# Kernel optimization log

Measured on AMD Instinct MI355X. Metric: run time of the kernel, lower is better.

Reference implementation:

```python
import jax, jax.numpy as jnp
import numpy as np

IOU_THRESHOLD = 0.5
NEGATIVE_RATIO = 3
ALPHA = 1.0
B, A, D, G = 64, 8732, 85, 32  # batch, anchors, 4+81 classes, max gt per image


def cxcywh_to_xyxy(b):
    cx, cy, w, h = b[..., 0], b[..., 1], b[..., 2], b[..., 3]
    return jnp.stack([cx - w / 2, cy - h / 2, cx + w / 2, cy + h / 2], axis=-1)


def box_iou(a, b):
    # a: (G,4) xyxy, b: (A,4) xyxy -> (G,A)
    lt = jnp.maximum(a[:, None, :2], b[None, :, :2])
    rb = jnp.minimum(a[:, None, 2:], b[None, :, 2:])
    wh = jnp.clip(rb - lt, 0.0)
    inter = wh[..., 0] * wh[..., 1]
    area_a = (a[:, 2] - a[:, 0]) * (a[:, 3] - a[:, 1])
    area_b = (b[:, 2] - b[:, 0]) * (b[:, 3] - b[:, 1])
    return inter / (area_a[:, None] + area_b[None, :] - inter)


def encode(gt, anchors):
    g_cxcy = (gt[:, :2] - anchors[:, :2]) / anchors[:, 2:]
    g_wh = jnp.log(gt[:, 2:]) - jnp.log(anchors[:, 2:])
    return jnp.concatenate([g_cxcy, g_wh], axis=-1)


def match_one(gt_box, gt_label, count, anchors):
    # gt_box (G,4) cxcywh, gt_label (G,), count scalar, anchors (A,4) cxcywh
    num_anchors = anchors.shape[0]
    valid = jnp.arange(gt_box.shape[0]) < count
    iou = box_iou(cxcywh_to_xyxy(gt_box), cxcywh_to_xyxy(anchors))  # (G,A)
    iou = jnp.where(valid[:, None], iou, -1.0)
    best_gt_overlap = iou.max(0)
    best_gt_idx = iou.argmax(0)
    over = best_gt_overlap > IOU_THRESHOLD
    loc = jnp.where(over[:, None], encode(gt_box[best_gt_idx], anchors), 0.0)
    cls = jnp.where(over, gt_label[best_gt_idx].astype(jnp.float32) + 1.0, 0.0)
    # force-match: each (valid) gt claims its best anchor, overwriting
    best_prior_idx = iou.argmax(1)  # (G,)
    idx = jnp.where(valid, best_prior_idx, num_anchors)  # dump invalid gt into a scratch row
    loc = jnp.concatenate([loc, jnp.zeros((1, 4), loc.dtype)], 0)
    loc = loc.at[idx].set(encode(gt_box, anchors[best_prior_idx]))[:num_anchors]
    cls = jnp.concatenate([cls, jnp.zeros((1,), cls.dtype)], 0)
    cls = cls.at[idx].set(gt_label.astype(jnp.float32) + 1.0)[:num_anchors]
    return loc, cls


def smooth_l1(d):
    ad = jnp.abs(d)
    return jnp.where(ad < 1.0, 0.5 * d * d, ad - 0.5)


def multibox_loss(pred, anchors, gt_boxes, gt_labels, gt_counts):
    num_anchors = pred.shape[1]
    loc_pred, conf_pred = pred[:, :, :4], pred[:, :, 4:]
    target_loc, target_cls = jax.vmap(match_one, in_axes=(0, 0, 0, None))(
        gt_boxes, gt_labels, gt_counts, anchors)  # (B,A,4), (B,A)
    pos = target_cls > 0  # (B,A)
    posf = pos.astype(pred.dtype)
    n_pos = posf.sum(1)  # (B,) guaranteed > 0 since every image has >=1 gt
    # localization: per-element smooth-L1 on positives, normalized per image
    loc_l = smooth_l1(loc_pred - target_loc) * posf[:, :, None]
    loc_loss = jnp.sum(loc_l / n_pos[:, None, None])
    # classification CE per anchor
    logp = jax.nn.log_softmax(conf_pred, axis=-1)  # (B,A,C)
    cls_ce = -jnp.take_along_axis(logp, target_cls.astype(jnp.int32)[:, :, None], axis=-1)[..., 0]
    pos_loss = jnp.sum(cls_ce * posf / n_pos[:, None])
    # hard negative mining (double-sort rank trick, no grad through selection)
    num_neg = jnp.minimum(NEGATIVE_RATIO * pos.sum(1), num_anchors - 1)  # (B,) int
    all_neg = jax.lax.stop_gradient(jnp.where(pos, 0.0, cls_ce))
    order = jnp.argsort(-all_neg, axis=1)
    rank = jnp.argsort(order, axis=1)
    neg_mask = (rank < num_neg[:, None]).astype(pred.dtype)
    neg_ce = -logp[:, :, 0]  # CE against background class 0
    neg_loss = jnp.sum(neg_ce * neg_mask / n_pos[:, None])
    return ALPHA * loc_loss + pos_loss + neg_loss


def setup_inputs() -> dict:
    key = jax.random.key(0)
    k1, k2, k3, k4, k5, k6, k7 = jax.random.split(key, 7)
    pred = jax.random.normal(k1, (B, A, D), dtype=jnp.float32)
    anchors = jnp.concatenate([
        jax.random.uniform(k2, (A, 2), minval=0.0, maxval=1.0),
        jax.random.uniform(k3, (A, 2), minval=0.05, maxval=0.5)], axis=-1)
    gt_boxes = jnp.concatenate([
        jax.random.uniform(k4, (B, G, 2), minval=0.0, maxval=1.0),
        jax.random.uniform(k5, (B, G, 2), minval=0.05, maxval=0.6)], axis=-1)
    gt_labels = jax.random.randint(k6, (B, G), 0, 80)
    gt_counts = jax.random.randint(k7, (B,), 1, G + 1)
    return {"pred": pred, "anchors": anchors, "gt_boxes": gt_boxes,
            "gt_labels": gt_labels, "gt_counts": gt_counts}


def reference(pred, anchors, gt_boxes, gt_labels, gt_counts):
    return multibox_loss(pred, anchors, gt_boxes, gt_labels, gt_counts)
```

## Files before the change

### kernel.cpp

```cpp
#include <hip/hip_runtime.h>
#include <math.h>

#define BB 64
#define AA 8732
#define DD 85
#define GG 32
#define CC 81
#define TILE 64
#define RPB 4
#define NLB 35
#define NSB GG


typedef __attribute__((address_space(3))) unsigned int lds_u32;
typedef const __attribute__((address_space(1))) unsigned int glb_u32;

__device__ __forceinline__ float smoothl1(float d) {
  float ad = fabsf(d);
  return ad < 1.0f ? 0.5f * d * d : ad - 0.5f;
}

__device__ __forceinline__ float frcp(float x) {
  return __builtin_amdgcn_rcpf(x);
}

__global__ __launch_bounds__(256) void k_fused(
    const float* __restrict__ pred, const float* __restrict__ anchors,
    const float* __restrict__ gt_boxes, const int* __restrict__ gt_labels,
    const int* __restrict__ gt_counts, float* __restrict__ all_neg,
    float* __restrict__ partials, int* __restrict__ poscnts,
    int* __restrict__ bestp, unsigned* __restrict__ epoch)
{
  const int b = blockIdx.y;
  const int tid = threadIdx.x;
  const int cnt = gt_counts[b];

  __shared__ float sgx0[GG], sgy0[GG], sgx1[GG], sgy1[GG], sgar[GG];
  __shared__ float4 sgb[GG];
  __shared__ int slab[GG];
  __shared__ float wsum[4];
  __shared__ int wcnt[4];

  if (blockIdx.x < NLB) {
    if (blockIdx.x == 0 && b == 0 && tid == 0) *epoch = 0u;
    if (tid < GG) {
      float4 gb = reinterpret_cast<const float4*>(gt_boxes)[b * GG + tid];
      sgb[tid] = gb;
      float x0 = gb.x - gb.z * 0.5f, y0 = gb.y - gb.w * 0.5f;
      float x1 = gb.x + gb.z * 0.5f, y1 = gb.y + gb.w * 0.5f;
      sgx0[tid] = x0; sgy0[tid] = y0; sgx1[tid] = x1; sgy1[tid] = y1;
      sgar[tid] = (x1 - x0) * (y1 - y0);
      slab[tid] = gt_labels[b * GG + tid];
    }
    __syncthreads();

    const int abase = blockIdx.x * RPB * TILE;
    const int r = tid >> 2;
    const int sub = tid & 3;
    float acc = 0.0f;
    int poscnt = 0;

    for (int i = 0; i < RPB; ++i) {
      const int a0 = abase + i * TILE;
      if (a0 >= AA) break;
      const int a = a0 + r;
      if (a < AA) {
        const float* base = pred + ((size_t)b * AA + a) * DD;
        float4 s0 = *(const float4*)(base + (sub)      * 4);
        float4 s1 = *(const float4*)(base + (sub + 4)  * 4);
        float4 s2 = *(const float4*)(base + (sub + 8)  * 4);
        float4 s3 = *(const float4*)(base + (sub + 12) * 4);
        float4 s4 = *(const float4*)(base + (sub + 16) * 4);
        float4 s5f = make_float4(0.f, 0.f, 0.f, 0.f);
        float  s5x = 0.0f;
        if (sub == 0) s5f = *(const float4*)(base + 80);
        if (sub == 1) s5x = base[84];
        float4 an = reinterpret_cast<const float4*>(anchors)[a];

        float ax0 = an.x - an.z * 0.5f, ay0 = an.y - an.w * 0.5f;
        float ax1 = an.x + an.z * 0.5f, ay1 = an.y + an.w * 0.5f;
        float aar = (ax1 - ax0) * (ay1 - ay0);
        float bv = -1.0f; int bg = 0;
        for (int g = sub; g < cnt; g += 4) {
          float iw = fmaxf(fminf(sgx1[g], ax1) - fmaxf(sgx0[g], ax0), 0.0f);
          float ih = fmaxf(fminf(sgy1[g], ay1) - fmaxf(sgy0[g], ay0), 0.0f);
          float inter = iw * ih;
          float iou = inter * frcp(sgar[g] + aar - inter);
          if (iou > bv) { bv = iou; bg = g; }
        }
        #pragma unroll
        for (int msk = 1; msk <= 2; msk <<= 1) {
          float ov = __shfl_xor(bv, msk);
          int   og = __shfl_xor(bg, msk);
          if (ov > bv || (ov == bv && og < bg)) { bv = ov; bg = og; }
        }
        const int m = (bv > 0.5f) ? bg : -1;
        const int tgt = (m >= 0) ? slab[m] + 1 : 0;

        const int cb = 4 * sub - 4;
        float mx = -INFINITY, xt = -INFINITY;
        #define SCAN(v, ccb)                                                 \
          { mx = fmaxf(fmaxf(fmaxf(mx, (v).x), (v).y), fmaxf((v).z, (v).w)); \
            if ((ccb) + 0 == tgt) xt = (v).x;                                \
            if ((ccb) + 1 == tgt) xt = (v).y;                                \
            if ((ccb) + 2 == tgt) xt = (v).z;                                \
            if ((ccb) + 3 == tgt) xt = (v).w; }
        if (sub > 0) SCAN(s0, cb);
        SCAN(s1, cb + 16); SCAN(s2, cb + 32); SCAN(s3, cb + 48); SCAN(s4, cb + 64);
        if (sub == 0) SCAN(s5f, 76);
        if (sub == 1) { mx = fmaxf(mx, s5x); if (tgt == 80) xt = s5x; }
        #undef SCAN
        #pragma unroll
        for (int msk = 1; msk <= 2; msk <<= 1)
          mx = fmaxf(mx, __shfl_xor(mx, msk));

        float s = 0.0f;
        #define ESUM(v) s += __expf((v).x - mx) + __expf((v).y - mx) +        \
                             __expf((v).z - mx) + __expf((v).w - mx);
        if (sub > 0) ESUM(s0);
        ESUM(s1); ESUM(s2); ESUM(s3); ESUM(s4);
        if (sub == 0) ESUM(s5f);
        if (sub == 1) s += __expf(s5x - mx);
        #undef ESUM
        #pragma unroll
        for (int msk = 1; msk <= 2; msk <<= 1) {
          s  += __shfl_xor(s, msk);
          xt  = fmaxf(xt, __shfl_xor(xt, msk));
        }
        const float lse = mx + __logf(s);
        const float ce = lse - xt;

        if (sub == 0) {
          if (m >= 0) {
            poscnt += 1;
            float4 gb = sgb[m];
            float tx = (gb.x - an.x) / an.z;
            float ty = (gb.y - an.y) / an.w;
            float tw = __logf(gb.z) - __logf(an.z);
            float th = __logf(gb.w) - __logf(an.w);
            acc += smoothl1(s0.x - tx) + smoothl1(s0.y - ty)
                 + smoothl1(s0.z - tw) + smoothl1(s0.w - th) + ce;
            all_neg[b * AA + a] = 0.0f;
          } else {
            all_neg[b * AA + a] = fmaxf(ce, 0.0f);
          }
        }
      }
    }

    #pragma unroll
    for (int msk = 1; msk < 64; msk <<= 1) {
      acc    += __shfl_xor(acc, msk);
      poscnt += __shfl_xor(poscnt, msk);
    }
    if ((tid & 63) == 0) { wsum[tid >> 6] = acc; wcnt[tid >> 6] = poscnt; }
    __syncthreads();
    if (tid == 0) {
      partials[b * NLB + blockIdx.x] = (wsum[0] + wsum[1]) + (wsum[2] + wsum[3]);
      poscnts[b * NLB + blockIdx.x] = wcnt[0] + wcnt[1] + wcnt[2] + wcnt[3];
    }
  } else {
    const int g = blockIdx.x - NLB;
    if (g >= cnt) return;

    float4 gb = reinterpret_cast<const float4*>(gt_boxes)[b * GG + g];
    const float gx0s = gb.x - gb.z * 0.5f, gy0s = gb.y - gb.w * 0.5f;
    const float gx1s = gb.x + gb.z * 0.5f, gy1s = gb.y + gb.w * 0.5f;
    const float gars = (gx1s - gx0s) * (gy1s - gy0s);

    float bv = -2.0f; int bi = AA;
    for (int a = tid; a < AA; a += 256) {
      float4 an = reinterpret_cast<const float4*>(anchors)[a];
      float ax0 = an.x - an.z * 0.5f, ay0 = an.y - an.w * 0.5f;
      float ax1 = an.x + an.z * 0.5f, ay1 = an.y + an.w * 0.5f;
      float aar = (ax1 - ax0) * (ay1 - ay0);
      float iw = fmaxf(fminf(gx1s, ax1) - fmaxf(gx0s, ax0), 0.0f);
      float ih = fmaxf(fminf(gy1s, ay1) - fmaxf(gy0s, ay0), 0.0f);
      float inter = iw * ih;
      float iou = inter * frcp(gars + aar - inter);
      if (iou > bv || (iou == bv && a < bi)) { bv = iou; bi = a; }
    }
    #pragma unroll
    for (int m = 1; m < 64; m <<= 1) {
      float ov = __shfl_xor(bv, m);
      int   oi = __shfl_xor(bi, m);
      if (ov > bv || (ov == bv && oi < bi)) { bv = ov; bi = oi; }
    }
    if ((tid & 63) == 0) { wsum[tid >> 6] = bv; wcnt[tid >> 6] = bi; }
    __syncthreads();
    if (tid == 0) {
      float fv = wsum[0]; int fi = wcnt[0];
      #pragma unroll
      for (int w = 1; w < 4; ++w)
        if (wsum[w] > fv || (wsum[w] == fv && wcnt[w] < fi)) { fv = wsum[w]; fi = wcnt[w]; }
      bestp[b * GG + g] = fi;
    }
  }
}

__global__ __launch_bounds__(1024) void k_select(
    const float* __restrict__ pred, const float* __restrict__ anchors,
    const float* __restrict__ gt_boxes, const int* __restrict__ gt_labels,
    const int* __restrict__ gt_counts, const float* __restrict__ all_neg,
    const float* __restrict__ partials, const int* __restrict__ poscnts,
    const int* __restrict__ bestp, float* __restrict__ batch_total,
    unsigned* __restrict__ epoch, float* __restrict__ out)
{
  const int b = blockIdx.x;
  const int tid = threadIdx.x;
  __shared__ unsigned u[AA];
  __shared__ int hist16[16][257];
  __shared__ int hist[256];
  __shared__ float sgx0[GG], sgy0[GG], sgx1[GG], sgy1[GG], sgar[GG];
  __shared__ float4 sgb[GG];
  __shared__ int slab[GG];
  __shared__ float sdelta[GG];
  __shared__ int sdnp[GG];
  __shared__ unsigned sh_pref;
  __shared__ int sh_k;
  __shared__ int sh_np;
  __shared__ float sh_base;
  __shared__ int sflag;
  __shared__ float wf[16];
  __shared__ int wc[16];

  {
    const float* srcg = all_neg + (size_t)b * AA;
    #pragma unroll
    for (int j = 0; j < 3; ++j) {
      int c = j * 1024 + tid;
      if (c < 2183)
        __builtin_amdgcn_global_load_lds(
            (glb_u32*)(srcg + c * 4), (lds_u32*)((float*)u + c * 4), 16, 0, 0);
    }
  }
  if (tid < GG) {
    float4 gb = reinterpret_cast<const float4*>(gt_boxes)[b * GG + tid];
    sgb[tid] = gb;
    float x0 = gb.x - gb.z * 0.5f, y0 = gb.y - gb.w * 0.5f;
    float x1 = gb.x + gb.z * 0.5f, y1 = gb.y + gb.w * 0.5f;
    sgx0[tid] = x0; sgy0[tid] = y0; sgx1[tid] = x1; sgy1[tid] = y1;
    sgar[tid] = (x1 - x0) * (y1 - y0);
    slab[tid] = gt_labels[b * GG + tid];
    sdelta[tid] = 0.0f; sdnp[tid] = 0;
  }

  float ps = 0.0f; int pc = 0;
  if (tid < 64) {
    float pv = (tid < NLB) ? partials[b * NLB + tid] : 0.0f;
    int   cv = (tid < NLB) ? poscnts[b * NLB + tid] : 0;
    #pragma unroll
    for (int m = 1; m < 64; m <<= 1) { pv += __shfl_xor(pv, m); cv += __shfl_xor(cv, m); }
    ps = pv; pc = cv;
  }
  __syncthreads();

  const int cnt = gt_counts[b];
  if (tid < cnt) {
    const int g = tid;
    const int p = bestp[b * GG + g];
    bool last = true;
    for (int g2 = g + 1; g2 < cnt; ++g2)
      if (bestp[b * GG + g2] == p) last = false;
    if (last) {
      const float* row = pred + ((size_t)b * AA + p) * DD;
      float mx = -INFINITY;
      for (int c = 0; c < CC; ++c) mx = fmaxf(mx, row[4 + c]);
      float s = 0.0f;
      for (int c = 0; c < CC; ++c) s += __expf(row[4 + c] - mx);
      const float lse = mx + __logf(s);
      float4 an = reinterpret_cast<const float4*>(anchors)[p];
      float ax0 = an.x - an.z * 0.5f, ay0 = an.y - an.w * 0.5f;
      float ax1 = an.x + an.z * 0.5f, ay1 = an.y + an.w * 0.5f;
      float aar = (ax1 - ax0) * (ay1 - ay0);
      float bv = -1.0f; int bg = 0;
      for (int g2 = 0; g2 < cnt; ++g2) {
        float iw = fmaxf(fminf(sgx1[g2], ax1) - fmaxf(sgx0[g2], ax0), 0.0f);
        float ih = fmaxf(fminf(sgy1[g2], ay1) - fmaxf(sgy0[g2], ay0), 0.0f);
        float inter = iw * ih;
        float iou = inter * frcp(sgar[g2] + aar - inter);
        if (iou > bv) { bv = iou; bg = g2; }
      }
      const int m_old = (bv > 0.5f) ? bg : -1;

      auto posterm = [&](int m) -> float {
        const int tgt = slab[m] + 1;
        float ce = lse - row[4 + tgt];
        float4 gb = sgb[m];
        float tx = (gb.x - an.x) / an.z;
        float ty = (gb.y - an.y) / an.w;
        float tw = __logf(gb.z) - __logf(an.z);
        float th = __logf(gb.w) - __logf(an.w);
        return smoothl1(row[0] - tx) + smoothl1(row[1] - ty)
             + smoothl1(row[2] - tw) + smoothl1(row[3] - th) + ce;
      };
      float delta = posterm(g) - ((m_old >= 0) ? posterm(m_old) : 0.0f);
      sdelta[g] = delta;
      sdnp[g] = (m_old < 0) ? 1 : 0;
      u[p] = 0u;
    }
  }
  __syncthreads();

  if (tid == 0) {
    float dl = 0.0f; int dn = 0;
    for (int g = 0; g < cnt; ++g) { dl += sdelta[g]; dn += sdnp[g]; }
    const int npf = pc + dn;
    sh_np = npf;
    sh_base = ps + dl;
    sh_k = min(3 * npf, AA - 1);
  }
  __syncthreads();

  const int np = sh_np;
  const int wvid = tid >> 6;

  unsigned prefix = 0;
  int kk = sh_k;
  for (int shift = 24; shift >= 0; shift -= 8) {
    int* hflat = &hist16[0][0];
    for (int i = tid; i < 16 * 257; i += 1024) hflat[i] = 0;
    __syncthreads();
    const unsigned hmask = (shift == 24) ? 0u : (0xFFFFFFFFu << (shift + 8));
    for (int i = tid; i < AA; i += 1024) {
      unsigned x = u[i];
      if ((x & hmask) == prefix)
        atomicAdd(&hist16[wvid][(x >> shift) & 255], 1);
    }
    __syncthreads();
    if (tid < 256) {
      int s = 0;
      #pragma unroll
      for (int h = 0; h < 16; ++h) s += hist16[h][tid];
      hist[tid] = s;
    }
    __syncthreads();
    if (tid < 64) {
      int h0 = hist[4 * tid], h1 = hist[4 * tid + 1];
      int h2 = hist[4 * tid + 2], h3 = hist[4 * tid + 3];
      int lsum = h0 + h1 + h2 + h3;
      int suf = lsum;
      #pragma unroll
      for (int off = 1; off < 64; off <<= 1) {
        int o = __shfl_down(suf, off);
        suf += (tid + off < 64) ? o : 0;
      }
      int after = suf - lsum;
      int s3 = h3 + after, s2 = h2 + s3, s1 = h1 + s2, s0 = h0 + s1;
      if (s0 >= kk && s1 < kk)    { sh_pref = prefix | ((unsigned)(4*tid+0) << shift); sh_k = kk - s1; }
      if (s1 >= kk && s2 < kk)    { sh_pref = prefix | ((unsigned)(4*tid+1) << shift); sh_k = kk - s2; }
      if (s2 >= kk && s3 < kk)    { sh_pref = prefix | ((unsigned)(4*tid+2) << shift); sh_k = kk - s3; }
      if (s3 >= kk && after < kk) { sh_pref = prefix | ((unsigned)(4*tid+3) << shift); sh_k = kk - after; }
    }
    __syncthreads();
    prefix = sh_pref;
    kk = sh_k;
    __syncthreads();
  }
  const float tstar = __uint_as_float(prefix);
  const int K = min(3 * np, AA - 1);

  float ssum = 0.0f; int cgt = 0;
  for (int i = tid; i < AA; i += 1024) {
    float x = __uint_as_float(u[i]);
    if (x > tstar) { ssum += x; cgt += 1; }
  }
  #pragma unroll
  for (int m = 1; m < 64; m <<= 1) {
    ssum += __shfl_xor(ssum, m);
    cgt  += __shfl_xor(cgt, m);
  }
  if ((tid & 63) == 0) { wf[wvid] = ssum; wc[wvid] = cgt; }
  __syncthreads();
  if (tid == 0) {
    float S = 0.0f; int Cg = 0;
    #pragma unroll
    for (int w = 0; w < 16; ++w) { S += wf[w]; Cg += wc[w]; }
    float neg_sum = S + (float)(K - Cg) * tstar;
    batch_total[b] = (sh_base + neg_sum) / (float)np;
    __threadfence();
    unsigned old = atomicAdd(epoch, 1u);
    sflag = (old == (unsigned)(BB - 1)) ? 1 : 0;
  }
  __syncthreads();

  if (sflag) {
    __threadfence();
    if (tid < 64) {
      float v = batch_total[tid];
      #pragma unroll
      for (int m = 1; m < 64; m <<= 1) v += __shfl_xor(v, m);
      if (tid == 0) out[0] = v;
    }
  }
}

extern "C" void kernel_launch(void* const* d_in, const int* in_sizes, int n_in,
                              void* d_out, int out_size, void* d_ws, size_t ws_size,
                              hipStream_t stream) {
  (void)in_sizes; (void)n_in; (void)out_size; (void)ws_size;
  const float* pred      = (const float*)d_in[0];
  const float* anchors   = (const float*)d_in[1];
  const float* gt_boxes  = (const float*)d_in[2];
  const int*   gt_labels = (const int*)d_in[3];
  const int*   gt_counts = (const int*)d_in[4];

  char* ws = (char*)d_ws;
  float*    all_neg     = (float*)(ws + 0);
  float*    partials    = (float*)(ws + 2235392);
  int*      poscnts     = (int*)(ws + 2244352);
  float*    batch_total = (float*)(ws + 2253312);
  int*      bestp       = (int*)(ws + 2253568);
  unsigned* epoch       = (unsigned*)(ws + 2261760);
  float* out = (float*)d_out;

  hipLaunchKernelGGL(k_fused, dim3(NLB + NSB, BB), dim3(256), 0, stream,
                     pred, anchors, gt_boxes, gt_labels, gt_counts,
                     all_neg, partials, poscnts, bestp, epoch);
  hipLaunchKernelGGL(k_select, dim3(BB), dim3(1024), 0, stream,
                     pred, anchors, gt_boxes, gt_labels, gt_counts,
                     all_neg, partials, poscnts, bestp, batch_total, epoch, out);
}
```

Baseline: 89.84 us.

## Split anchor-to-gt matching into a separate kernel writing a match buffer

```diff
diff --git a/kernel.cpp b/kernel.cpp
--- a/kernel.cpp
+++ b/kernel.cpp
@@ -9,7 +9,6 @@
 #define TILE 64
 #define RPB 4
 #define NLB 35
-#define NSB GG
 
 
 typedef __attribute__((address_space(3))) unsigned int lds_u32;
@@ -24,32 +23,60 @@
   return __builtin_amdgcn_rcpf(x);
 }
 
-__global__ __launch_bounds__(256) void k_fused(
+__global__ __launch_bounds__(256) void k_A(
+    const float* __restrict__ anchors, const float* __restrict__ gt_boxes,
+    const int* __restrict__ gt_counts, int* __restrict__ match,
+    unsigned* __restrict__ epoch)
+{
+  const int b = blockIdx.y;
+  const int count = gt_counts[b];
+  __shared__ float gx0[GG], gy0[GG], gx1[GG], gy1[GG], gar[GG];
+
+  if (blockIdx.x == 0 && b == 0 && threadIdx.x == 0) *epoch = 0u;
+  if (threadIdx.x < GG) {
+    float4 gb = reinterpret_cast<const float4*>(gt_boxes)[b * GG + threadIdx.x];
+    float x0 = gb.x - gb.z * 0.5f, y0 = gb.y - gb.w * 0.5f;
+    float x1 = gb.x + gb.z * 0.5f, y1 = gb.y + gb.w * 0.5f;
+    gx0[threadIdx.x] = x0; gy0[threadIdx.x] = y0;
+    gx1[threadIdx.x] = x1; gy1[threadIdx.x] = y1;
+    gar[threadIdx.x] = (x1 - x0) * (y1 - y0);
+  }
+  __syncthreads();
+  const int a = blockIdx.x * 256 + threadIdx.x;
+  if (a >= AA) return;
+
+  float4 an = reinterpret_cast<const float4*>(anchors)[a];
+  float ax0 = an.x - an.z * 0.5f, ay0 = an.y - an.w * 0.5f;
+  float ax1 = an.x + an.z * 0.5f, ay1 = an.y + an.w * 0.5f;
+  float aar = (ax1 - ax0) * (ay1 - ay0);
+  float best = -1.0f; int bi = 0;
+  for (int g = 0; g < count; ++g) {
+    float iw = fmaxf(fminf(gx1[g], ax1) - fmaxf(gx0[g], ax0), 0.0f);
+    float ih = fmaxf(fminf(gy1[g], ay1) - fmaxf(gy0[g], ay0), 0.0f);
+    float inter = iw * ih;
+    float iou = inter * frcp(gar[g] + aar - inter);
+    if (iou > best) { best = iou; bi = g; }
+  }
+  match[b * AA + a] = (best > 0.5f) ? bi : -1;
+}
+
+__global__ __launch_bounds__(256) void k_B(
     const float* __restrict__ pred, const float* __restrict__ anchors,
     const float* __restrict__ gt_boxes, const int* __restrict__ gt_labels,
-    const int* __restrict__ gt_counts, float* __restrict__ all_neg,
-    float* __restrict__ partials, int* __restrict__ poscnts,
-    int* __restrict__ bestp, unsigned* __restrict__ epoch)
+    const int* __restrict__ gt_counts, const int* __restrict__ match,
+    float* __restrict__ all_neg, float* __restrict__ partials,
+    int* __restrict__ poscnts, int* __restrict__ bestp)
 {
   const int b = blockIdx.y;
   const int tid = threadIdx.x;
-  const int cnt = gt_counts[b];
-
-  __shared__ float sgx0[GG], sgy0[GG], sgx1[GG], sgy1[GG], sgar[GG];
   __shared__ float4 sgb[GG];
   __shared__ int slab[GG];
   __shared__ float wsum[4];
   __shared__ int wcnt[4];
 
   if (blockIdx.x < NLB) {
-    if (blockIdx.x == 0 && b == 0 && tid == 0) *epoch = 0u;
     if (tid < GG) {
-      float4 gb = reinterpret_cast<const float4*>(gt_boxes)[b * GG + tid];
-      sgb[tid] = gb;
-      float x0 = gb.x - gb.z * 0.5f, y0 = gb.y - gb.w * 0.5f;
-      float x1 = gb.x + gb.z * 0.5f, y1 = gb.y + gb.w * 0.5f;
-      sgx0[tid] = x0; sgy0[tid] = y0; sgx1[tid] = x1; sgy1[tid] = y1;
-      sgar[tid] = (x1 - x0) * (y1 - y0);
+      sgb[tid] = reinterpret_cast<const float4*>(gt_boxes)[b * GG + tid];
       slab[tid] = gt_labels[b * GG + tid];
     }
     __syncthreads();
@@ -75,26 +102,8 @@
         float  s5x = 0.0f;
         if (sub == 0) s5f = *(const float4*)(base + 80);
         if (sub == 1) s5x = base[84];
-        float4 an = reinterpret_cast<const float4*>(anchors)[a];
-
-        float ax0 = an.x - an.z * 0.5f, ay0 = an.y - an.w * 0.5f;
-        float ax1 = an.x + an.z * 0.5f, ay1 = an.y + an.w * 0.5f;
-        float aar = (ax1 - ax0) * (ay1 - ay0);
-        float bv = -1.0f; int bg = 0;
-        for (int g = sub; g < cnt; g += 4) {
-          float iw = fmaxf(fminf(sgx1[g], ax1) - fmaxf(sgx0[g], ax0), 0.0f);
-          float ih = fmaxf(fminf(sgy1[g], ay1) - fmaxf(sgy0[g], ay0), 0.0f);
-          float inter = iw * ih;
-          float iou = inter * frcp(sgar[g] + aar - inter);
-          if (iou > bv) { bv = iou; bg = g; }
-        }
-        #pragma unroll
-        for (int msk = 1; msk <= 2; msk <<= 1) {
-          float ov = __shfl_xor(bv, msk);
-          int   og = __shfl_xor(bg, msk);
-          if (ov > bv || (ov == bv && og < bg)) { bv = ov; bg = og; }
-        }
-        const int m = (bv > 0.5f) ? bg : -1;
+
+        const int m = match[b * AA + a];
         const int tgt = (m >= 0) ? slab[m] + 1 : 0;
 
         const int cb = 4 * sub - 4;
@@ -133,6 +142,7 @@
         if (sub == 0) {
           if (m >= 0) {
             poscnt += 1;
+            float4 an = reinterpret_cast<const float4*>(anchors)[a];
             float4 gb = sgb[m];
             float tx = (gb.x - an.x) / an.z;
             float ty = (gb.y - an.y) / an.w;
@@ -161,7 +171,7 @@
     }
   } else {
     const int g = blockIdx.x - NLB;
-    if (g >= cnt) return;
+    if (g >= gt_counts[b]) return;
 
     float4 gb = reinterpret_cast<const float4*>(gt_boxes)[b * GG + g];
     const float gx0s = gb.x - gb.z * 0.5f, gy0s = gb.y - gb.w * 0.5f;
@@ -198,20 +208,20 @@
   }
 }
 
-__global__ __launch_bounds__(1024) void k_select(
+__global__ __launch_bounds__(1024) void k_C(
     const float* __restrict__ pred, const float* __restrict__ anchors,
     const float* __restrict__ gt_boxes, const int* __restrict__ gt_labels,
-    const int* __restrict__ gt_counts, const float* __restrict__ all_neg,
-    const float* __restrict__ partials, const int* __restrict__ poscnts,
-    const int* __restrict__ bestp, float* __restrict__ batch_total,
-    unsigned* __restrict__ epoch, float* __restrict__ out)
+    const int* __restrict__ gt_counts, const int* __restrict__ match,
+    const float* __restrict__ all_neg, const float* __restrict__ partials,
+    const int* __restrict__ poscnts, const int* __restrict__ bestp,
+    float* __restrict__ batch_total, unsigned* __restrict__ epoch,
+    float* __restrict__ out)
 {
   const int b = blockIdx.x;
   const int tid = threadIdx.x;
   __shared__ unsigned u[AA];
   __shared__ int hist16[16][257];
   __shared__ int hist[256];
-  __shared__ float sgx0[GG], sgy0[GG], sgx1[GG], sgy1[GG], sgar[GG];
   __shared__ float4 sgb[GG];
   __shared__ int slab[GG];
   __shared__ float sdelta[GG];
@@ -235,12 +245,7 @@
     }
   }
   if (tid < GG) {
-    float4 gb = reinterpret_cast<const float4*>(gt_boxes)[b * GG + tid];
-    sgb[tid] = gb;
-    float x0 = gb.x - gb.z * 0.5f, y0 = gb.y - gb.w * 0.5f;
-    float x1 = gb.x + gb.z * 0.5f, y1 = gb.y + gb.w * 0.5f;
-    sgx0[tid] = x0; sgy0[tid] = y0; sgx1[tid] = x1; sgy1[tid] = y1;
-    sgar[tid] = (x1 - x0) * (y1 - y0);
+    sgb[tid] = reinterpret_cast<const float4*>(gt_boxes)[b * GG + tid];
     slab[tid] = gt_labels[b * GG + tid];
     sdelta[tid] = 0.0f; sdnp[tid] = 0;
   }
@@ -263,6 +268,7 @@
     for (int g2 = g + 1; g2 < cnt; ++g2)
       if (bestp[b * GG + g2] == p) last = false;
     if (last) {
+      const int m_old = match[b * AA + p];
       const float* row = pred + ((size_t)b * AA + p) * DD;
       float mx = -INFINITY;
       for (int c = 0; c < CC; ++c) mx = fmaxf(mx, row[4 + c]);
@@ -270,18 +276,6 @@
       for (int c = 0; c < CC; ++c) s += __expf(row[4 + c] - mx);
       const float lse = mx + __logf(s);
       float4 an = reinterpret_cast<const float4*>(anchors)[p];
-      float ax0 = an.x - an.z * 0.5f, ay0 = an.y - an.w * 0.5f;
-      float ax1 = an.x + an.z * 0.5f, ay1 = an.y + an.w * 0.5f;
-      float aar = (ax1 - ax0) * (ay1 - ay0);
-      float bv = -1.0f; int bg = 0;
-      for (int g2 = 0; g2 < cnt; ++g2) {
-        float iw = fmaxf(fminf(sgx1[g2], ax1) - fmaxf(sgx0[g2], ax0), 0.0f);
-        float ih = fmaxf(fminf(sgy1[g2], ay1) - fmaxf(sgy0[g2], ay0), 0.0f);
-        float inter = iw * ih;
-        float iou = inter * frcp(sgar[g2] + aar - inter);
-        if (iou > bv) { bv = iou; bg = g2; }
-      }
-      const int m_old = (bv > 0.5f) ? bg : -1;
 
       auto posterm = [&](int m) -> float {
         const int tgt = slab[m] + 1;
@@ -294,8 +288,7 @@
         return smoothl1(row[0] - tx) + smoothl1(row[1] - ty)
              + smoothl1(row[2] - tw) + smoothl1(row[3] - th) + ce;
       };
-      float delta = posterm(g) - ((m_old >= 0) ? posterm(m_old) : 0.0f);
-      sdelta[g] = delta;
+      sdelta[g] = posterm(g) - ((m_old >= 0) ? posterm(m_old) : 0.0f);
       sdnp[g] = (m_old < 0) ? 1 : 0;
       u[p] = 0u;
     }
@@ -406,18 +399,21 @@
   const int*   gt_counts = (const int*)d_in[4];
 
   char* ws = (char*)d_ws;
-  float*    all_neg     = (float*)(ws + 0);
-  float*    partials    = (float*)(ws + 2235392);
-  int*      poscnts     = (int*)(ws + 2244352);
-  float*    batch_total = (float*)(ws + 2253312);
-  int*      bestp       = (int*)(ws + 2253568);
-  unsigned* epoch       = (unsigned*)(ws + 2261760);
+  int*      match       = (int*)(ws + 0);
+  float*    all_neg     = (float*)(ws + 2235392);
+  float*    partials    = (float*)(ws + 4470784);
+  int*      poscnts     = (int*)(ws + 4479744);
+  float*    batch_total = (float*)(ws + 4488704);
+  int*      bestp       = (int*)(ws + 4488960);
+  unsigned* epoch       = (unsigned*)(ws + 4497152);
   float* out = (float*)d_out;
 
-  hipLaunchKernelGGL(k_fused, dim3(NLB + NSB, BB), dim3(256), 0, stream,
-                     pred, anchors, gt_boxes, gt_labels, gt_counts,
-                     all_neg, partials, poscnts, bestp, epoch);
-  hipLaunchKernelGGL(k_select, dim3(BB), dim3(1024), 0, stream,
-                     pred, anchors, gt_boxes, gt_labels, gt_counts,
+  hipLaunchKernelGGL(k_A, dim3(NLB, BB), dim3(256), 0, stream,
+                     anchors, gt_boxes, gt_counts, match, epoch);
+  hipLaunchKernelGGL(k_B, dim3(NLB + GG, BB), dim3(256), 0, stream,
+                     pred, anchors, gt_boxes, gt_labels, gt_counts, match,
+                     all_neg, partials, poscnts, bestp);
+  hipLaunchKernelGGL(k_C, dim3(BB), dim3(1024), 0, stream,
+                     pred, anchors, gt_boxes, gt_labels, gt_counts, match,
                      all_neg, partials, poscnts, bestp, batch_total, epoch, out);
 }
```

Measured after the change: 90.69 us. Within noise of the previous version (+1.0%).
